# Performance work log

Measured on AMD Instinct MI355X. Metric: run time of the kernel, lower is better.

Reference implementation:

```python
import jax, jax.numpy as jnp
import numpy as np

SEP_THRESHOLD = 5.0
TEMPERATURE = 0.1          # sigmoid temperature
SCALING_FACTOR = 1.0
DIST_TEMPERATURE = 1.0     # exponential temperature for repulsion energy
ATT_LOSS_GATE = 0.0
REP_LOSS_GATE = 0.0
EPS = 1e-10


def setup_inputs() -> dict:
    key = jax.random.key(0)
    k1, k2 = jax.random.split(key)
    B, L, K, C, D = 16, 64, 32, 32, 512
    prior = jax.random.normal(k1, (B, L, K, C), dtype=jnp.float32)
    h = jax.random.normal(k2, (B, L, D), dtype=jnp.float32)
    return {"prior": prior, "h": h}


def _jsd_matrix(prior):
    # prior: (B, L, K, C) logits -> pairwise JSD summed over K factors: (B, L, L)
    logp = jax.nn.log_softmax(prior, axis=-1)          # (B,L,K,C)
    p = jnp.exp(logp)
    p1, p2 = p[:, :, None], p[:, None]                  # (B,L,1,K,C), (B,1,L,K,C)
    lp1, lp2 = logp[:, :, None], logp[:, None]
    logm = jnp.log(0.5 * (p1 + p2))                     # mixture log-probs
    kl_p_m = jnp.sum(p1 * (lp1 - logm), axis=-1)        # (B,L,L,K)
    kl_q_m = jnp.sum(p2 * (lp2 - logm), axis=-1)
    jsd = 0.5 * (kl_p_m + kl_q_m)
    return jsd.sum(axis=-1) * SCALING_FACTOR            # (B,L,L)


def _ste_mask(soft, hard, triu):
    # straight-through: hard values forward, soft gradient backward
    return (hard + soft - jax.lax.stop_gradient(soft)) * triu


def reference(prior, h):
    B, L, K, C = prior.shape
    jsd = _jsd_matrix(prior)                            # (B,L,L)

    triu = jnp.triu(jnp.ones((L, L), dtype=prior.dtype), k=1)
    soft_att = jax.nn.sigmoid((SEP_THRESHOLD - jsd) / TEMPERATURE)
    hard_att = (jsd < SEP_THRESHOLD).astype(prior.dtype)
    att_mask = _ste_mask(soft_att, hard_att, triu)
    soft_rep = jax.nn.sigmoid((jsd - SEP_THRESHOLD) / TEMPERATURE)
    hard_rep = (jsd >= SEP_THRESHOLD).astype(prior.dtype)
    rep_mask = _ste_mask(soft_rep, hard_rep, triu)

    # pairwise MSE over hidden dim: (B,L,L)
    diff = h[:, :, None, :] - h[:, None, :, :]
    pairwise_mse = jnp.mean(diff * diff, axis=-1)

    loss_att = (pairwise_mse * att_mask).sum() / (att_mask.sum() + EPS)
    loss_att = jnp.where(loss_att > ATT_LOSS_GATE, loss_att, 0.0)

    repulsion_energy = jnp.exp(-pairwise_mse / DIST_TEMPERATURE)
    loss_rep = (repulsion_energy * rep_mask).sum() / (rep_mask.sum() + EPS)
    loss_rep = jnp.where(loss_rep > REP_LOSS_GATE, loss_rep, 0.0)

    return loss_att, loss_rep
```

## Files before the change

### kernel.cpp

```cpp
#include <hip/hip_runtime.h>
#include <math.h>

#define NB 16
#define NL 64
#define NK 32
#define NC 32
#define ND 512
#define EPSF 1e-10f

#define TILES_PER_B 36
#define PAIR_BLOCKS (NB * TILES_PER_B)

#define THRS 14.426950408889634f
#define L2E  1.4426950408889634f

typedef _Float16 half2v __attribute__((ext_vector_type(2)));
typedef _Float16 half4v __attribute__((ext_vector_type(4)));
typedef _Float16 half8v __attribute__((ext_vector_type(8)));


__global__ void __launch_bounds__(256) softmax_kernel(
        const float* __restrict__ prior,
        const float* __restrict__ hg,
        _Float16* __restrict__ P,
        float* __restrict__ H2,
        _Float16* __restrict__ h16) {
    int bl = blockIdx.x;
    int t  = threadIdx.x;

    const float* src = prior + (size_t)bl * (NK * NC);
    float4 x = *(const float4*)(src + t * 4);
    float y0 = x.x * L2E, y1 = x.y * L2E, y2 = x.z * L2E, y3 = x.w * L2E;

    float m = fmaxf(fmaxf(y0, y1), fmaxf(y2, y3));
    #pragma unroll
    for (int w = 4; w >= 1; w >>= 1)
        m = fmaxf(m, __shfl_xor(m, w, 8));

    float e0 = exp2f(y0 - m), e1 = exp2f(y1 - m);
    float e2 = exp2f(y2 - m), e3 = exp2f(y3 - m);
    float s = e0 + e1 + e2 + e3;
    #pragma unroll
    for (int w = 4; w >= 1; w >>= 1)
        s += __shfl_xor(s, w, 8);

    float rs = 1.0f / s;
    float ls = __log2f(s);
    float p0 = e0 * rs, p1 = e1 * rs, p2 = e2 * rs, p3 = e3 * rs;
    float l0 = (y0 - m) - ls, l1 = (y1 - m) - ls;
    float l2 = (y2 - m) - ls, l3 = (y3 - m) - ls;

    half4v pv;
    pv[0] = (_Float16)fmaxf(p0, 1e-6f);
    pv[1] = (_Float16)fmaxf(p1, 1e-6f);
    pv[2] = (_Float16)fmaxf(p2, 1e-6f);
    pv[3] = (_Float16)fmaxf(p3, 1e-6f);
    *(half4v*)(P + (size_t)bl * (NK * NC) + t * 4) = pv;

    float2 hv = *(const float2*)(hg + (size_t)bl * ND + t * 2);
    half2v hh; hh[0] = (_Float16)hv.x; hh[1] = (_Float16)hv.y;
    *(half2v*)(h16 + (size_t)bl * ND + t * 2) = hh;

    float hacc = p0 * l0 + p1 * l1 + p2 * l2 + p3 * l3;
    #pragma unroll
    for (int w = 32; w >= 1; w >>= 1)
        hacc += __shfl_xor(hacc, w);
    __shared__ float red[4];
    int lane = t & 63, wib = t >> 6;
    if (lane == 0) red[wib] = hacc;
    __syncthreads();
    if (t == 0) H2[bl] = red[0] + red[1] + red[2] + red[3];
}

__global__ void __launch_bounds__(512) pair_kernel(
        const _Float16* __restrict__ P,
        const float* __restrict__ H2g,
        const _Float16* __restrict__ h16,
        float* __restrict__ partials) {
    __shared__ _Float16 sP[2][8][1024];
    __shared__ _Float16 sH[2][8][512];
    __shared__ float sh2j[8];
    __shared__ float red[8][4];

    int tid  = threadIdx.x;
    int lane = tid & 63;
    int wv   = tid >> 6;

    int b   = blockIdx.x / TILES_PER_B;
    int t36 = blockIdx.x % TILES_PER_B;
    int ti = 0, rem = t36;
    while (rem >= 8 - ti) { rem -= 8 - ti; ++ti; }
    int tj = ti + rem;
    bool diag = (ti == tj);
    int bi0 = b * NL + ti * 8;
    int bj0 = b * NL + tj * 8;

    {
        const float4* sp = (const float4*)(P + (size_t)bi0 * (NK * NC));
        float4* dp = (float4*)&sP[0][0][0];
        dp[tid] = sp[tid]; dp[tid + 512] = sp[tid + 512];
        const float4* sh = (const float4*)(h16 + (size_t)bi0 * ND);
        ((float4*)&sH[0][0][0])[tid] = sh[tid];
    }
    if (!diag) {
        const float4* sp = (const float4*)(P + (size_t)bj0 * (NK * NC));
        float4* dp = (float4*)&sP[1][0][0];
        dp[tid] = sp[tid]; dp[tid + 512] = sp[tid + 512];
        const float4* sh = (const float4*)(h16 + (size_t)bj0 * ND);
        ((float4*)&sH[1][0][0])[tid] = sh[tid];
    }
    if (tid < 8) sh2j[tid] = H2g[bj0 + tid];
    __syncthreads();

    int gj = diag ? 0 : 1;
    int r  = wv;

    half8v ar1 = *(const half8v*)&sP[0][r][lane * 8];
    half8v ar2 = *(const half8v*)&sP[0][r][512 + lane * 8];
    half8v hr  = *(const half8v*)&sH[0][r][lane * 8];
    float h2i = H2g[bi0 + r];

    bool hi32 = (lane & 32) != 0;
    bool hi16 = (lane & 16) != 0;
    int  smine_base = lane >> 4;

    float attN = 0.0f, attC = 0.0f, repN = 0.0f, repC = 0.0f;

    #pragma unroll
    for (int sb = 0; sb < 8; sb += 4) {
        float S[4], M[4];
        #pragma unroll
        for (int q = 0; q < 4; ++q) {
            int s = sb + q;
            half8v b1 = *(const half8v*)&sP[gj][s][lane * 8];
            half8v t1 = ar1 + b1;
            half8v b2 = *(const half8v*)&sP[gj][s][512 + lane * 8];
            half8v t2 = ar2 + b2;
            float a0 = 0.f, a1 = 0.f;
            #pragma unroll
            for (int e = 0; e < 8; ++e) {
                float f = (float)t1[e]; a0 = fmaf(f, __log2f(f), a0);
                float g = (float)t2[e]; a1 = fmaf(g, __log2f(g), a1);
            }
            S[q] = a0 + a1;

            half8v hs = *(const half8v*)&sH[gj][s][lane * 8];
            half8v d = hr - hs;
            float m0 = 0.f, m1 = 0.f;
            #pragma unroll
            for (int e = 0; e < 8; e += 2) {
                m0 = fmaf((float)d[e],     (float)d[e],     m0);
                m1 = fmaf((float)d[e + 1], (float)d[e + 1], m1);
            }
            M[q] = m0 + m1;
        }

        float sel0 = hi32 ? S[2] : S[0], oth0 = hi32 ? S[0] : S[2];
        float sel1 = hi32 ? S[3] : S[1], oth1 = hi32 ? S[1] : S[3];
        float w0 = sel0 + __shfl_xor(oth0, 32);
        float w1 = sel1 + __shfl_xor(oth1, 32);
        float selS = hi16 ? w1 : w0, othS = hi16 ? w0 : w1;
        float xS = selS + __shfl_xor(othS, 16);
        xS += __shfl_xor(xS, 8);
        xS += __shfl_xor(xS, 4);
        xS += __shfl_xor(xS, 2);
        xS += __shfl_xor(xS, 1);

        float mel0 = hi32 ? M[2] : M[0], mot0 = hi32 ? M[0] : M[2];
        float mel1 = hi32 ? M[3] : M[1], mot1 = hi32 ? M[1] : M[3];
        float u0 = mel0 + __shfl_xor(mot0, 32);
        float u1 = mel1 + __shfl_xor(mot1, 32);
        float selM = hi16 ? u1 : u0, othM = hi16 ? u0 : u1;
        float xM = selM + __shfl_xor(othM, 16);
        xM += __shfl_xor(xM, 8);
        xM += __shfl_xor(xM, 4);
        xM += __shfl_xor(xM, 2);
        xM += __shfl_xor(xM, 1);

        int s = sb + smine_base;
        float stat = h2i + sh2j[s] + 64.0f - xS;
        float mse  = xM * (1.0f / ND);
        float rterm = exp2f(-mse * L2E);
        bool valid = (!diag) || (s > r);
        bool act   = ((lane & 15) == 0) && valid;
        bool isAtt = stat < THRS;
        attN += (act && isAtt)  ? mse   : 0.0f;
        attC += (act && isAtt)  ? 1.0f  : 0.0f;
        repN += (act && !isAtt) ? rterm : 0.0f;
        repC += (act && !isAtt) ? 1.0f  : 0.0f;
    }

    attN += __shfl_xor(attN, 16); attN += __shfl_xor(attN, 32);
    attC += __shfl_xor(attC, 16); attC += __shfl_xor(attC, 32);
    repN += __shfl_xor(repN, 16); repN += __shfl_xor(repN, 32);
    repC += __shfl_xor(repC, 16); repC += __shfl_xor(repC, 32);

    if (lane == 0) {
        red[wv][0] = attN; red[wv][1] = attC;
        red[wv][2] = repN; red[wv][3] = repC;
    }
    __syncthreads();
    if (tid < 4) {
        float v = 0.0f;
        #pragma unroll
        for (int w = 0; w < 8; ++w) v += red[w][tid];
        partials[blockIdx.x * 4 + tid] = v;
    }
}

__global__ void __launch_bounds__(256) finalize_kernel(
        const float* __restrict__ partials,
        float* __restrict__ out) {
    int tid = threadIdx.x;
    float a0 = 0.0f, a1 = 0.0f, a2 = 0.0f, a3 = 0.0f;
    for (int bkt = tid; bkt < PAIR_BLOCKS; bkt += 256) {
        a0 += partials[bkt * 4 + 0];
        a1 += partials[bkt * 4 + 1];
        a2 += partials[bkt * 4 + 2];
        a3 += partials[bkt * 4 + 3];
    }
    #pragma unroll
    for (int w = 32; w >= 1; w >>= 1) {
        a0 += __shfl_xor(a0, w);
        a1 += __shfl_xor(a1, w);
        a2 += __shfl_xor(a2, w);
        a3 += __shfl_xor(a3, w);
    }
    __shared__ float red[4][4];
    int lane = tid & 63, wib = tid >> 6;
    if (lane == 0) {
        red[wib][0] = a0; red[wib][1] = a1; red[wib][2] = a2; red[wib][3] = a3;
    }
    __syncthreads();
    if (tid == 0) {
        float s0 = red[0][0] + red[1][0] + red[2][0] + red[3][0];
        float s1 = red[0][1] + red[1][1] + red[2][1] + red[3][1];
        float s2 = red[0][2] + red[1][2] + red[2][2] + red[3][2];
        float s3 = red[0][3] + red[1][3] + red[2][3] + red[3][3];
        float la = s0 / (s1 + EPSF);
        float lr = s2 / (s3 + EPSF);
        out[0] = (la > 0.0f) ? la : 0.0f;
        out[1] = (lr > 0.0f) ? lr : 0.0f;
    }
}

extern "C" void kernel_launch(void* const* d_in, const int* in_sizes, int n_in,
                              void* d_out, int out_size, void* d_ws, size_t ws_size,
                              hipStream_t stream) {
    const float* prior = (const float*)d_in[0];
    const float* h     = (const float*)d_in[1];
    float* out = (float*)d_out;
    float* ws  = (float*)d_ws;

    float* partials = ws;
    _Float16* P = (_Float16*)(ws + 4096);
    float* H2 = ws + 4096 + 524288;
    _Float16* h16 = (_Float16*)(ws + 4096 + 524288 + 1024);

    softmax_kernel<<<NB * NL, 256, 0, stream>>>(prior, h, P, H2, h16);

    pair_kernel<<<PAIR_BLOCKS, 512, 0, stream>>>(P, H2, h16, partials);

    finalize_kernel<<<1, 256, 0, stream>>>(partials, out);
}
```

Measured before the change: 26.94 us.

## Split pair tiles across two workgroups and early-exit second-half JSD

Each 8x8 pair tile now runs as two 256-thread workgroups, each handling four i-rows, which doubles the grid and cuts per-block shared memory. The per-row entropy term H2 is stored as two halves over factors K. The pairwise JSD statistic is first computed over the first 16 factors. The second half is computed only if some valid pair in the wave could still fall below the threshold, relying on each factor's JSD being non-negative. This aims to skip log2 work and improve CU occupancy, at the cost of a wave-divergent branch and the j-tile being loaded redundantly by both halves.

```diff
diff --git a/kernel.cpp b/kernel.cpp
--- a/kernel.cpp
+++ b/kernel.cpp
@@ -9,7 +9,7 @@
 #define EPSF 1e-10f
 
 #define TILES_PER_B 36
-#define PAIR_BLOCKS (NB * TILES_PER_B)
+#define PAIR_BLOCKS (NB * TILES_PER_B * 2)
 
 #define THRS 14.426950408889634f
 #define L2E  1.4426950408889634f
@@ -23,7 +23,7 @@
         const float* __restrict__ prior,
         const float* __restrict__ hg,
         _Float16* __restrict__ P,
-        float* __restrict__ H2,
+        float2* __restrict__ H2,
         _Float16* __restrict__ h16) {
     int bl = blockIdx.x;
     int t  = threadIdx.x;
@@ -69,25 +69,47 @@
     int lane = t & 63, wib = t >> 6;
     if (lane == 0) red[wib] = hacc;
     __syncthreads();
-    if (t == 0) H2[bl] = red[0] + red[1] + red[2] + red[3];
-}
-
-__global__ void __launch_bounds__(512) pair_kernel(
+    if (t == 0)
+        H2[bl] = make_float2(red[0] + red[1], red[2] + red[3]);
+}
+
+__device__ __forceinline__ float bf4(float v0, float v1, float v2, float v3,
+                                     bool hi32, bool hi16) {
+    float sel0 = hi32 ? v2 : v0, oth0 = hi32 ? v0 : v2;
+    float sel1 = hi32 ? v3 : v1, oth1 = hi32 ? v1 : v3;
+    float w0 = sel0 + __shfl_xor(oth0, 32);
+    float w1 = sel1 + __shfl_xor(oth1, 32);
+    float sel = hi16 ? w1 : w0, oth = hi16 ? w0 : w1;
+    float x = sel + __shfl_xor(oth, 16);
+    x += __shfl_xor(x, 8);
+    x += __shfl_xor(x, 4);
+    x += __shfl_xor(x, 2);
+    x += __shfl_xor(x, 1);
+    return x;
+}
+
+__global__ void __launch_bounds__(256) pair_kernel(
         const _Float16* __restrict__ P,
-        const float* __restrict__ H2g,
+        const float2* __restrict__ H2g,
         const _Float16* __restrict__ h16,
         float* __restrict__ partials) {
-    __shared__ _Float16 sP[2][8][1024];
-    __shared__ _Float16 sH[2][8][512];
-    __shared__ float sh2j[8];
-    __shared__ float red[8][4];
+    __shared__ _Float16 sPj[8][1024];
+    __shared__ _Float16 sHj[8][512];
+    __shared__ _Float16 sPi[4][1024];
+    __shared__ _Float16 sHi[4][512];
+    __shared__ float2 sh2j[8];
+    __shared__ float red[4][4];
 
     int tid  = threadIdx.x;
     int lane = tid & 63;
     int wv   = tid >> 6;
 
-    int b   = blockIdx.x / TILES_PER_B;
-    int t36 = blockIdx.x % TILES_PER_B;
+    int wg    = blockIdx.x;
+    int b     = wg / (TILES_PER_B * 2);
+    int rem72 = wg % (TILES_PER_B * 2);
+    int t36   = rem72 >> 1;
+    int half  = rem72 & 1;
+
     int ti = 0, rem = t36;
     while (rem >= 8 - ti) { rem -= 8 - ti; ++ti; }
     int tj = ti + rem;
@@ -96,33 +118,37 @@
     int bj0 = b * NL + tj * 8;
 
     {
-        const float4* sp = (const float4*)(P + (size_t)bi0 * (NK * NC));
-        float4* dp = (float4*)&sP[0][0][0];
-        dp[tid] = sp[tid]; dp[tid + 512] = sp[tid + 512];
-        const float4* sh = (const float4*)(h16 + (size_t)bi0 * ND);
-        ((float4*)&sH[0][0][0])[tid] = sh[tid];
+        const float4* sp = (const float4*)(P + (size_t)bj0 * (NK * NC));
+        float4* dp = (float4*)&sPj[0][0];
+        #pragma unroll
+        for (int k = 0; k < 4; ++k) dp[tid + 256 * k] = sp[tid + 256 * k];
+        const float4* sh = (const float4*)(h16 + (size_t)bj0 * ND);
+        float4* dh = (float4*)&sHj[0][0];
+        dh[tid] = sh[tid]; dh[tid + 256] = sh[tid + 256];
     }
     if (!diag) {
-        const float4* sp = (const float4*)(P + (size_t)bj0 * (NK * NC));
-        float4* dp = (float4*)&sP[1][0][0];
-        dp[tid] = sp[tid]; dp[tid + 512] = sp[tid + 512];
-        const float4* sh = (const float4*)(h16 + (size_t)bj0 * ND);
-        ((float4*)&sH[1][0][0])[tid] = sh[tid];
+        int bihalf = bi0 + half * 4;
+        const float4* sp = (const float4*)(P + (size_t)bihalf * (NK * NC));
+        float4* dp = (float4*)&sPi[0][0];
+        dp[tid] = sp[tid]; dp[tid + 256] = sp[tid + 256];
+        const float4* sh = (const float4*)(h16 + (size_t)bihalf * ND);
+        ((float4*)&sHi[0][0])[tid] = sh[tid];
     }
     if (tid < 8) sh2j[tid] = H2g[bj0 + tid];
     __syncthreads();
 
-    int gj = diag ? 0 : 1;
-    int r  = wv;
-
-    half8v ar1 = *(const half8v*)&sP[0][r][lane * 8];
-    half8v ar2 = *(const half8v*)&sP[0][r][512 + lane * 8];
-    half8v hr  = *(const half8v*)&sH[0][r][lane * 8];
-    float h2i = H2g[bi0 + r];
+    int r = half * 4 + wv;
+
+    const _Float16* arow = diag ? &sPj[r][0] : &sPi[wv][0];
+    const _Float16* hrow = diag ? &sHj[r][0] : &sHi[wv][0];
+    half8v ar1 = *(const half8v*)&arow[lane * 8];
+    half8v ar2 = *(const half8v*)&arow[512 + lane * 8];
+    half8v hr  = *(const half8v*)&hrow[lane * 8];
+    float2 h2i = H2g[bi0 + r];
 
     bool hi32 = (lane & 32) != 0;
     bool hi16 = (lane & 16) != 0;
-    int  smine_base = lane >> 4;
+    int  sgrp = lane >> 4;
 
     float attN = 0.0f, attC = 0.0f, repN = 0.0f, repC = 0.0f;
 
@@ -132,19 +158,17 @@
         #pragma unroll
         for (int q = 0; q < 4; ++q) {
             int s = sb + q;
-            half8v b1 = *(const half8v*)&sP[gj][s][lane * 8];
+            half8v b1 = *(const half8v*)&sPj[s][lane * 8];
             half8v t1 = ar1 + b1;
-            half8v b2 = *(const half8v*)&sP[gj][s][512 + lane * 8];
-            half8v t2 = ar2 + b2;
             float a0 = 0.f, a1 = 0.f;
             #pragma unroll
-            for (int e = 0; e < 8; ++e) {
-                float f = (float)t1[e]; a0 = fmaf(f, __log2f(f), a0);
-                float g = (float)t2[e]; a1 = fmaf(g, __log2f(g), a1);
+            for (int e = 0; e < 8; e += 2) {
+                float f0 = (float)t1[e];     a0 = fmaf(f0, __log2f(f0), a0);
+                float f1 = (float)t1[e + 1]; a1 = fmaf(f1, __log2f(f1), a1);
             }
             S[q] = a0 + a1;
 
-            half8v hs = *(const half8v*)&sH[gj][s][lane * 8];
+            half8v hs = *(const half8v*)&sHj[s][lane * 8];
             half8v d = hr - hs;
             float m0 = 0.f, m1 = 0.f;
             #pragma unroll
@@ -155,33 +179,36 @@
             M[q] = m0 + m1;
         }
 
-        float sel0 = hi32 ? S[2] : S[0], oth0 = hi32 ? S[0] : S[2];
-        float sel1 = hi32 ? S[3] : S[1], oth1 = hi32 ? S[1] : S[3];
-        float w0 = sel0 + __shfl_xor(oth0, 32);
-        float w1 = sel1 + __shfl_xor(oth1, 32);
-        float selS = hi16 ? w1 : w0, othS = hi16 ? w0 : w1;
-        float xS = selS + __shfl_xor(othS, 16);
-        xS += __shfl_xor(xS, 8);
-        xS += __shfl_xor(xS, 4);
-        xS += __shfl_xor(xS, 2);
-        xS += __shfl_xor(xS, 1);
-
-        float mel0 = hi32 ? M[2] : M[0], mot0 = hi32 ? M[0] : M[2];
-        float mel1 = hi32 ? M[3] : M[1], mot1 = hi32 ? M[1] : M[3];
-        float u0 = mel0 + __shfl_xor(mot0, 32);
-        float u1 = mel1 + __shfl_xor(mot1, 32);
-        float selM = hi16 ? u1 : u0, othM = hi16 ? u0 : u1;
-        float xM = selM + __shfl_xor(othM, 16);
-        xM += __shfl_xor(xM, 8);
-        xM += __shfl_xor(xM, 4);
-        xM += __shfl_xor(xM, 2);
-        xM += __shfl_xor(xM, 1);
-
-        int s = sb + smine_base;
-        float stat = h2i + sh2j[s] + 64.0f - xS;
-        float mse  = xM * (1.0f / ND);
+        float xSA = bf4(S[0], S[1], S[2], S[3], hi32, hi16);
+        float xM  = bf4(M[0], M[1], M[2], M[3], hi32, hi16);
+
+        int smine = sb + sgrp;
+        float2 h2j = sh2j[smine];
+        float statA = h2i.x + h2j.x + 32.0f - xSA;
+        bool valid = (!diag) || (smine > r);
+        float stat = statA;
+
+        if (__any(valid && (statA < THRS))) {
+            float SB[4];
+            #pragma unroll
+            for (int q = 0; q < 4; ++q) {
+                int s = sb + q;
+                half8v b2 = *(const half8v*)&sPj[s][512 + lane * 8];
+                half8v t2 = ar2 + b2;
+                float a0 = 0.f, a1 = 0.f;
+                #pragma unroll
+                for (int e = 0; e < 8; e += 2) {
+                    float g0 = (float)t2[e];     a0 = fmaf(g0, __log2f(g0), a0);
+                    float g1 = (float)t2[e + 1]; a1 = fmaf(g1, __log2f(g1), a1);
+                }
+                SB[q] = a0 + a1;
+            }
+            float xSB = bf4(SB[0], SB[1], SB[2], SB[3], hi32, hi16);
+            stat = statA + (h2i.y + h2j.y + 32.0f - xSB);
+        }
+
+        float mse   = xM * (1.0f / ND);
         float rterm = exp2f(-mse * L2E);
-        bool valid = (!diag) || (s > r);
         bool act   = ((lane & 15) == 0) && valid;
         bool isAtt = stat < THRS;
         attN += (act && isAtt)  ? mse   : 0.0f;
@@ -201,9 +228,7 @@
     }
     __syncthreads();
     if (tid < 4) {
-        float v = 0.0f;
-        #pragma unroll
-        for (int w = 0; w < 8; ++w) v += red[w][tid];
+        float v = red[0][tid] + red[1][tid] + red[2][tid] + red[3][tid];
         partials[blockIdx.x * 4 + tid] = v;
     }
 }
@@ -253,13 +278,13 @@
     float* ws  = (float*)d_ws;
 
     float* partials = ws;
-    _Float16* P = (_Float16*)(ws + 4096);
-    float* H2 = ws + 4096 + 524288;
-    _Float16* h16 = (_Float16*)(ws + 4096 + 524288 + 1024);
+    _Float16* P = (_Float16*)(ws + 8192);
+    float2* H2 = (float2*)(ws + 8192 + 524288);
+    _Float16* h16 = (_Float16*)(ws + 8192 + 524288 + 2048);
 
     softmax_kernel<<<NB * NL, 256, 0, stream>>>(prior, h, P, H2, h16);
 
-    pair_kernel<<<PAIR_BLOCKS, 512, 0, stream>>>(P, H2, h16, partials);
+    pair_kernel<<<PAIR_BLOCKS, 256, 0, stream>>>(P, H2, h16, partials);
 
     finalize_kernel<<<1, 256, 0, stream>>>(partials, out);
 }
```

Measured after the change: 25.46 us. 1.06x faster.
